# Kernel tuning notes

Measured on AMD Instinct MI355X. Metric: run time of the kernel, lower is better.

The kernel has to match this reference:

```python
import jax, jax.numpy as jnp
import numpy as np

B, N, D, H = 4, 8192, 1024, 16
HD = D // H  # head dim 64
EPS = 1e-5


def setup_inputs() -> dict:
    key = jax.random.key(0)
    ks = jax.random.split(key, 12)
    s = 1.0 / np.sqrt(D)
    return {
        "query": jax.random.normal(ks[0], (B, N, D), jnp.float32),
        "Wq": jax.random.normal(ks[1], (D, D), jnp.float32) * s,
        "bq": jax.random.normal(ks[2], (D,), jnp.float32) * 0.01,
        "Wk": jax.random.normal(ks[3], (D, D), jnp.float32) * s,
        "bk": jax.random.normal(ks[4], (D,), jnp.float32) * 0.01,
        "Wv": jax.random.normal(ks[5], (D, D), jnp.float32) * s,
        "bv": jax.random.normal(ks[6], (D,), jnp.float32) * 0.01,
        "Wu": jax.random.normal(ks[7], (D, D), jnp.float32) * s,
        "bu": jax.random.normal(ks[8], (D,), jnp.float32) * 0.01,
        "Wo": jax.random.normal(ks[9], (D, D), jnp.float32) * s,
        "bo": jax.random.normal(ks[10], (D,), jnp.float32) * 0.01,
        "ln_w": jnp.ones((D,), jnp.float32),
        "ln_b": jnp.zeros((D,), jnp.float32),
    }


def _abs_clamp(t, min_mag=0.01, max_mag=100.0):
    return jnp.clip(jnp.abs(t), min_mag, max_mag) * jnp.sign(t)


def _heads(x):  # [b, n, h*d] -> [b, h, n, d]
    b, n, _ = x.shape
    return x.reshape(b, n, H, HD).transpose(0, 2, 1, 3)


def reference(query, Wq, bq, Wk, bk, Wv, bv, Wu, bu, Wo, bo, ln_w, ln_b):
    q = jax.nn.relu(_heads(query @ Wq + bq))  # [b,h,n,d]
    k = jax.nn.relu(_heads(query @ Wk + bk))
    v = _heads(query @ Wv + bv)
    u = query @ Wu + bu  # [b,n,D]
    # global linear-attention reduction: kv[b,h,d,e] = sum_n k v
    kv = jnp.einsum('bhnd,bhne->bhde', k, v)
    kv = _abs_clamp(kv)
    out = jnp.einsum('bhnd,bhde->bhne', q, kv)  # [b,h,n,d]
    out = out.transpose(0, 2, 1, 3).reshape(query.shape)  # [b,n,D]
    # LayerNorm over last dim
    mu = jnp.mean(out, axis=-1, keepdims=True)
    var = jnp.var(out, axis=-1, keepdims=True)
    out = (out - mu) * jax.lax.rsqrt(var + EPS) * ln_w + ln_b
    out = u * out
    return out @ Wo + bo
```

## Files before the change

### kernel.cpp

```cpp
#include <hip/hip_runtime.h>

#define M_TOT 32768

typedef float f32x4 __attribute__((ext_vector_type(4)));
typedef short s16x8 __attribute__((ext_vector_type(8)));

#define AS1(p) ((__attribute__((address_space(1))) void*)(p))
#define AS3(p) ((__attribute__((address_space(3))) void*)(p))

#define BARRIER() asm volatile("s_barrier" ::: "memory")
#define VMCNT4() asm volatile("s_waitcnt vmcnt(4)" ::: "memory")
#define VMCNT2() asm volatile("s_waitcnt vmcnt(2)" ::: "memory")
#define VMCNT0() asm volatile("s_waitcnt vmcnt(0)" ::: "memory")

__device__ __forceinline__ short f2bf(float f) {
    unsigned u = __builtin_bit_cast(unsigned, f);
    u += 0x7fffu + ((u >> 16) & 1u);
    return (short)(u >> 16);
}
__device__ __forceinline__ float bf2f(short s) {
    unsigned u = ((unsigned)(unsigned short)s) << 16;
    return __builtin_bit_cast(float, u);
}

__global__ void conv_x(const float* __restrict__ x, short* __restrict__ y) {
    const size_t nchunk = (size_t)M_TOT * 1024 / 8;
    const size_t stride = (size_t)gridDim.x * blockDim.x;
    for (size_t c = (size_t)blockIdx.x * blockDim.x + threadIdx.x; c < nchunk; c += stride) {
        const float4* src = (const float4*)(x + c * 8);
        float4 a = src[0], b = src[1];
        s16x8 r;
        r[0] = f2bf(a.x); r[1] = f2bf(a.y); r[2] = f2bf(a.z); r[3] = f2bf(a.w);
        r[4] = f2bf(b.x); r[5] = f2bf(b.y); r[6] = f2bf(b.z); r[7] = f2bf(b.w);
        *(s16x8*)(y + c * 8) = r;
    }
}

__global__ void conv_w(const float* __restrict__ Wq, const float* __restrict__ Wk,
                       const float* __restrict__ Wv, const float* __restrict__ Wu,
                       const float* __restrict__ Wo, short* __restrict__ Wcat) {
    const int c = blockIdx.x * 256 + threadIdx.x;
    const int np = c >> 8;
    const int k0 = (c & 255) << 2;
    const float* W = (np < 1024) ? Wq : (np < 2048) ? Wk : (np < 3072) ? Wv
                   : (np < 4096) ? Wu : Wo;
    const int n = np & 1023;
    short4 r;
    r.x = f2bf(W[(size_t)(k0 + 0) * 1024 + n]);
    r.y = f2bf(W[(size_t)(k0 + 1) * 1024 + n]);
    r.z = f2bf(W[(size_t)(k0 + 2) * 1024 + n]);
    r.w = f2bf(W[(size_t)(k0 + 3) * 1024 + n]);
    *(short4*)(Wcat + (size_t)np * 1024 + k0) = r;
}

__global__ void conv_bias(const float* __restrict__ bq, const float* __restrict__ bk,
                          const float* __restrict__ bv, const float* __restrict__ bu,
                          const float* __restrict__ bo, float* __restrict__ bcat) {
    const int i = blockIdx.x * 256 + threadIdx.x;
    const float* b = (i < 1024) ? bq : (i < 2048) ? bk : (i < 3072) ? bv
                   : (i < 4096) ? bu : bo;
    bcat[i] = b[i & 1023];
}

template <int MODE>
__global__ __launch_bounds__(512, 2) void gemm8(
        const short* __restrict__ A, const short* __restrict__ W,
        const float* __restrict__ bias,
        short* __restrict__ qb, short* __restrict__ ktb,
        short* __restrict__ vtb, short* __restrict__ ub,
        float* __restrict__ outb) {
    extern __shared__ char lds[];
    const int tid = threadIdx.x;
    const int wave = tid >> 6, lane = tid & 63;
    const int r16 = lane & 15, g = lane >> 4;
    const int moff = (wave >> 2) << 7;
    const int noff = (wave & 3) << 6;

    const int nwg = (MODE == 0) ? 2048 : 512;
    const int NB = (MODE == 0) ? 16 : 4;
    const int bid = blockIdx.x;
    const int swz = (bid & 7) * (nwg >> 3) + (bid >> 3);
    const int mblk = swz / NB, nblk = swz % NB;
    const int row0 = mblk << 8, col0 = nblk << 8;

    const int rswz = r16 & 7;
    const int ck0 = (g ^ rswz) << 4;
    const int ck1 = ((4 + g) ^ rswz) << 4;
    const int rowbA = (moff + r16) << 7;
    const int rowbB = (noff + r16) << 7;

    const char* baseA = (const char*)A + (size_t)(row0 + wave * 8 + (lane >> 3)) * 2048
                        + (((lane & 7) ^ ((lane >> 3) & 7)) << 4);
    const char* baseB = (const char*)W + (size_t)(col0 + wave * 8 + (lane >> 3)) * 2048
                        + (((lane & 7) ^ ((lane >> 3) & 7)) << 4);

#define STG(BASE, J, T, DST)                                                   \
    __builtin_amdgcn_global_load_lds(                                          \
        AS1((BASE) + (size_t)(J) * 131072 + (size_t)(T) * 128),                \
        AS3((DST) + (J) * 8192 + wave * 1024), 16, 0, 0)

#define RDA(V, M, BUFA) {                                                      \
    (V)[0] = *(const s16x8*)((BUFA) + rowbA + (M) * 2048 + ck0);               \
    (V)[1] = *(const s16x8*)((BUFA) + rowbA + (M) * 2048 + ck1); }

#define RDB(V, N, BUFB) {                                                      \
    (V)[0] = *(const s16x8*)((BUFB) + rowbB + (N) * 2048 + ck0);               \
    (V)[1] = *(const s16x8*)((BUFB) + rowbB + (N) * 2048 + ck1); }

#define MF16(P)                                                                \
    _Pragma("unroll") for (int n = 0; n < 4; ++n) {                            \
        acc[2*(P)][n]   = __builtin_amdgcn_mfma_f32_16x16x32_bf16(afr[0][0], bfr[n][0], acc[2*(P)][n], 0, 0, 0);   \
        acc[2*(P)+1][n] = __builtin_amdgcn_mfma_f32_16x16x32_bf16(afr[1][0], bfr[n][0], acc[2*(P)+1][n], 0, 0, 0); \
        acc[2*(P)][n]   = __builtin_amdgcn_mfma_f32_16x16x32_bf16(afr[0][1], bfr[n][1], acc[2*(P)][n], 0, 0, 0);   \
        acc[2*(P)+1][n] = __builtin_amdgcn_mfma_f32_16x16x32_bf16(afr[1][1], bfr[n][1], acc[2*(P)+1][n], 0, 0, 0); \
    }

#define TILE(T, DOSTAGE, TR2, TR4) {                                           \
    char* bA_ = lds + ((T) & 1) * 65536; char* bB_ = bA_ + 32768;              \
    char* sA_ = lds + (((T) + 1) & 1) * 65536; char* sB_ = sA_ + 32768;        \
    s16x8 afr[2][2];                                                           \
    if (DOSTAGE) { STG(baseB, 0, (T) + 1, sB_); STG(baseB, 1, (T) + 1, sB_); } \
    _Pragma("unroll") for (int n = 0; n < 4; ++n) RDB(bfr[n], n, bB_);         \
    RDA(afr[0], 0, bA_); RDA(afr[1], 1, bA_);                                  \
    BARRIER(); __builtin_amdgcn_s_setprio(1); MF16(0);                         \
    __builtin_amdgcn_s_setprio(0); BARRIER();                                  \
    if (DOSTAGE) { STG(baseB, 2, (T) + 1, sB_); STG(baseB, 3, (T) + 1, sB_); } \
    RDA(afr[0], 2, bA_); RDA(afr[1], 3, bA_);                                  \
    BARRIER(); __builtin_amdgcn_s_setprio(1); MF16(1);                         \
    __builtin_amdgcn_s_setprio(0); TR2; BARRIER();                             \
    if (DOSTAGE) { STG(baseA, 0, (T) + 1, sA_); STG(baseA, 2, (T) + 1, sA_); } \
    RDA(afr[0], 4, bA_); RDA(afr[1], 5, bA_);                                  \
    BARRIER(); __builtin_amdgcn_s_setprio(1); MF16(2);                         \
    __builtin_amdgcn_s_setprio(0); BARRIER();                                  \
    if (DOSTAGE) { STG(baseA, 1, (T) + 1, sA_); STG(baseA, 3, (T) + 1, sA_); } \
    RDA(afr[0], 6, bA_); RDA(afr[1], 7, bA_);                                  \
    BARRIER(); __builtin_amdgcn_s_setprio(1); MF16(3);                         \
    __builtin_amdgcn_s_setprio(0); TR4; BARRIER();                             \
}

    f32x4 acc[8][4] = {};
    s16x8 bfr[4][2];

    STG(baseB, 0, 0, lds + 32768); STG(baseB, 1, 0, lds + 32768);
    STG(baseB, 2, 0, lds + 32768); STG(baseB, 3, 0, lds + 32768);
    STG(baseA, 0, 0, lds);         STG(baseA, 2, 0, lds);
    STG(baseA, 1, 0, lds);         STG(baseA, 3, 0, lds);
    VMCNT2();
    BARRIER();

    #pragma unroll 1
    for (int t = 0; t < 15; ++t) TILE(t, true, VMCNT4(), VMCNT2());
    TILE(15, false, VMCNT0(), (void)0);

    const int rj = (lane >> 4) << 2;
    if (MODE == 1) {
        #pragma unroll
        for (int n = 0; n < 4; ++n) {
            const int gn = col0 + noff + n * 16 + r16;
            const float bv = bias[gn];
            #pragma unroll
            for (int m = 0; m < 8; ++m) {
                const int gm0 = row0 + moff + m * 16 + rj;
                #pragma unroll
                for (int j = 0; j < 4; ++j)
                    outb[(size_t)(gm0 + j) * 1024 + gn] = acc[m][n][j] + bv;
            }
        }
    } else {
        const int seg = col0 >> 10;
        if (seg == 0 || seg == 3) {
            short* dst = (seg == 0) ? qb : ub;
            const bool do_relu = (seg == 0);
            #pragma unroll
            for (int n = 0; n < 4; ++n) {
                const int gn = col0 + noff + n * 16 + r16;
                const int f = gn & 1023;
                const float bv = bias[gn];
                #pragma unroll
                for (int m = 0; m < 8; ++m) {
                    const int gm0 = row0 + moff + m * 16 + rj;
                    #pragma unroll
                    for (int j = 0; j < 4; ++j) {
                        float val = acc[m][n][j] + bv;
                        if (do_relu) val = fmaxf(val, 0.0f);
                        dst[(size_t)(gm0 + j) * 1024 + f] = f2bf(val);
                    }
                }
            }
        } else {
            short* dst = (seg == 1) ? ktb : vtb;
            const bool do_relu = (seg == 1);
            #pragma unroll
            for (int n = 0; n < 4; ++n) {
                const int gn = col0 + noff + n * 16 + r16;
                const int hd = gn & 1023;
                const float bv = bias[gn];
                #pragma unroll
                for (int m = 0; m < 8; ++m) {
                    const int gm0 = row0 + moff + m * 16 + rj;
                    const int b = gm0 >> 13;
                    const int ntok = gm0 & 8191;
                    float v0 = acc[m][n][0] + bv, v1 = acc[m][n][1] + bv;
                    float v2 = acc[m][n][2] + bv, v3 = acc[m][n][3] + bv;
                    if (do_relu) {
                        v0 = fmaxf(v0, 0.0f); v1 = fmaxf(v1, 0.0f);
                        v2 = fmaxf(v2, 0.0f); v3 = fmaxf(v3, 0.0f);
                    }
                    short4 pk;
                    pk.x = f2bf(v0); pk.y = f2bf(v1); pk.z = f2bf(v2); pk.w = f2bf(v3);
                    *(short4*)(dst + ((size_t)(b * 1024 + hd)) * 8192 + ntok) = pk;
                }
            }
        }
    }
#undef TILE
#undef MF16
#undef RDB
#undef RDA
#undef STG
}

__global__ __launch_bounds__(64) void kv_partial(const short* __restrict__ ktb,
                                                 const short* __restrict__ vtb,
                                                 float* __restrict__ kvp) {
    const int slice = blockIdx.x;
    const int bh = blockIdx.y;
    const int lane = threadIdx.x;
    const int r16 = lane & 15;
    const short* kb = ktb + (size_t)bh * 64 * 8192;
    const short* vb = vtb + (size_t)bh * 64 * 8192;
    const int n0 = slice << 8;
    f32x4 acc[4][4] = {};
    for (int s = 0; s < 8; ++s) {
        const int nk = n0 + (s << 5) + ((lane >> 4) << 3);
        s16x8 af[4], bf[4];
        #pragma unroll
        for (int m = 0; m < 4; ++m) af[m] = *(const s16x8*)(kb + (size_t)(m * 16 + r16) * 8192 + nk);
        #pragma unroll
        for (int n = 0; n < 4; ++n) bf[n] = *(const s16x8*)(vb + (size_t)(n * 16 + r16) * 8192 + nk);
        #pragma unroll
        for (int m = 0; m < 4; ++m)
            #pragma unroll
            for (int n = 0; n < 4; ++n)
                acc[m][n] = __builtin_amdgcn_mfma_f32_16x16x32_bf16(af[m], bf[n], acc[m][n], 0, 0, 0);
    }
    float* dst = kvp + ((size_t)slice * 64 + bh) * 4096;
    const int rj = (lane >> 4) << 2;
    #pragma unroll
    for (int m = 0; m < 4; ++m)
        #pragma unroll
        for (int n = 0; n < 4; ++n)
            #pragma unroll
            for (int j = 0; j < 4; ++j)
                dst[(size_t)(m * 16 + rj + j) * 64 + n * 16 + r16] = acc[m][n][j];
}

__global__ void kv_reduce(const float* __restrict__ kvp, short* __restrict__ kvt) {
    const int bh = blockIdx.x;
    for (int i = threadIdx.x; i < 4096; i += 256) {
        float s = 0.0f;
        #pragma unroll 8
        for (int sl = 0; sl < 32; ++sl)
            s += kvp[((size_t)sl * 64 + bh) * 4096 + i];
        float a = fabsf(s);
        float cmag = fminf(fmaxf(a, 0.01f), 100.0f);
        float r = (s > 0.0f) ? cmag : ((s < 0.0f) ? -cmag : 0.0f);
        const int d = i >> 6, e = i & 63;
        kvt[(size_t)bh * 4096 + e * 64 + d] = f2bf(r);
    }
}

__global__ __launch_bounds__(256) void qkv_out(const short* __restrict__ qb,
                                               const short* __restrict__ kvt,
                                               float* __restrict__ ob) {
    const int bh = blockIdx.y;
    const int b = bh >> 4, h = bh & 15;
    const int tid = threadIdx.x;
    const int wave = tid >> 6, lane = tid & 63;
    const int r16 = lane & 15;
    const size_t mbase = (size_t)b * 8192 + ((size_t)blockIdx.x << 8) + (wave << 6);
    const short* kvb = kvt + (size_t)bh * 4096;
    f32x4 acc[4][4] = {};
    #pragma unroll
    for (int s = 0; s < 2; ++s) {
        const int kq2 = (s << 5) + ((lane >> 4) << 3);
        s16x8 af[4], bf[4];
        #pragma unroll
        for (int m = 0; m < 4; ++m)
            af[m] = *(const s16x8*)(qb + (mbase + m * 16 + r16) * 1024 + h * 64 + kq2);
        #pragma unroll
        for (int n = 0; n < 4; ++n)
            bf[n] = *(const s16x8*)(kvb + (n * 16 + r16) * 64 + kq2);
        #pragma unroll
        for (int m = 0; m < 4; ++m)
            #pragma unroll
            for (int n = 0; n < 4; ++n)
                acc[m][n] = __builtin_amdgcn_mfma_f32_16x16x32_bf16(af[m], bf[n], acc[m][n], 0, 0, 0);
    }
    const int rj = (lane >> 4) << 2;
    #pragma unroll
    for (int m = 0; m < 4; ++m)
        #pragma unroll
        for (int n = 0; n < 4; ++n)
            #pragma unroll
            for (int j = 0; j < 4; ++j)
                ob[(mbase + m * 16 + rj + j) * 1024 + h * 64 + n * 16 + r16] = acc[m][n][j];
}

__global__ __launch_bounds__(256) void ln_mul(const float* __restrict__ ob,
                                              const short* __restrict__ ub,
                                              const float* __restrict__ lnw,
                                              const float* __restrict__ lnb,
                                              short* __restrict__ yb) {
    const int row = blockIdx.x;
    const int tid = threadIdx.x;
    const float4 v = ((const float4*)(ob + (size_t)row * 1024))[tid];
    float s = v.x + v.y + v.z + v.w;
    float sq = v.x * v.x + v.y * v.y + v.z * v.z + v.w * v.w;
    #pragma unroll
    for (int off = 32; off > 0; off >>= 1) {
        s += __shfl_down(s, off);
        sq += __shfl_down(sq, off);
    }
    __shared__ float ls[4], lq[4];
    const int wave = tid >> 6, lane = tid & 63;
    if (lane == 0) { ls[wave] = s; lq[wave] = sq; }
    __syncthreads();
    const float S = ls[0] + ls[1] + ls[2] + ls[3];
    const float SQ = lq[0] + lq[1] + lq[2] + lq[3];
    const float mu = S * (1.0f / 1024.0f);
    const float var = SQ * (1.0f / 1024.0f) - mu * mu;
    const float rs = rsqrtf(var + 1e-5f);
    const short4 uu = ((const short4*)(ub + (size_t)row * 1024))[tid];
    const float4 w = ((const float4*)lnw)[tid];
    const float4 bb = ((const float4*)lnb)[tid];
    short4 o;
    o.x = f2bf(bf2f(uu.x) * ((v.x - mu) * rs * w.x + bb.x));
    o.y = f2bf(bf2f(uu.y) * ((v.y - mu) * rs * w.y + bb.y));
    o.z = f2bf(bf2f(uu.z) * ((v.z - mu) * rs * w.z + bb.z));
    o.w = f2bf(bf2f(uu.w) * ((v.w - mu) * rs * w.w + bb.w));
    ((short4*)(yb + (size_t)row * 1024))[tid] = o;
}

extern "C" void kernel_launch(void* const* d_in, const int* in_sizes, int n_in,
                              void* d_out, int out_size, void* d_ws, size_t ws_size,
                              hipStream_t stream) {
    (void)in_sizes; (void)n_in; (void)out_size;
    const float* query = (const float*)d_in[0];
    const float* Wq = (const float*)d_in[1];
    const float* bq = (const float*)d_in[2];
    const float* Wk = (const float*)d_in[3];
    const float* bk = (const float*)d_in[4];
    const float* Wv = (const float*)d_in[5];
    const float* bv = (const float*)d_in[6];
    const float* Wu = (const float*)d_in[7];
    const float* bu = (const float*)d_in[8];
    const float* Wo = (const float*)d_in[9];
    const float* bo = (const float*)d_in[10];
    const float* lnw = (const float*)d_in[11];
    const float* lnb = (const float*)d_in[12];
    float* out = (float*)d_out;
    char* ws = (char*)d_ws;
    if (ws_size < 380129280u) return;

    short* Xb   = (short*)(ws);
    short* Wcat = (short*)(ws + 67108864);
    float* bcat = (float*)(ws + 77594624);
    short* qb   = (short*)(ws + 77615104);
    short* ktb  = (short*)(ws + 144723968);
    short* vtb  = (short*)(ws + 211832832);
    short* ub   = (short*)(ws + 278941696);
    float* kvp  = (float*)(ws + 346050560);
    short* kvt  = (short*)(ws + 379604992);
    float* ob   = (float*)(ws + 144723968);
    short* yb   = Xb;

    hipFuncSetAttribute(reinterpret_cast<const void*>(&gemm8<0>),
                        hipFuncAttributeMaxDynamicSharedMemorySize, 131072);
    hipFuncSetAttribute(reinterpret_cast<const void*>(&gemm8<1>),
                        hipFuncAttributeMaxDynamicSharedMemorySize, 131072);

    conv_x<<<2048, 256, 0, stream>>>(query, Xb);
    conv_w<<<5120, 256, 0, stream>>>(Wq, Wk, Wv, Wu, Wo, Wcat);
    conv_bias<<<20, 256, 0, stream>>>(bq, bk, bv, bu, bo, bcat);
    gemm8<0><<<2048, 512, 131072, stream>>>(Xb, Wcat, bcat, qb, ktb, vtb, ub, nullptr);
    kv_partial<<<dim3(32, 64), 64, 0, stream>>>(ktb, vtb, kvp);
    kv_reduce<<<64, 256, 0, stream>>>(kvp, kvt);
    qkv_out<<<dim3(32, 64), 256, 0, stream>>>(qb, kvt, ob);
    ln_mul<<<32768, 256, 0, stream>>>(ob, ub, lnw, lnb, yb);
    gemm8<1><<<512, 512, 131072, stream>>>(yb, Wcat + (size_t)4096 * 1024, bcat + 4096,
                                           nullptr, nullptr, nullptr, nullptr, out);
}
```

Measured before the change: 600.5 us.

## Fuse q·kv product with LayerNorm and reduce kv partials inside blocks

Replaces the separate qkv_out and ln_mul kernels with one qkv_ln kernel. It computes each row's attention output per head with MFMA twice, once for the LayerNorm statistics and once for normalization, and then multiplies by u through an LDS transpose. This removes the fp32 round trip of the 128MB output buffer through global memory, at the cost of doing the small q·kv matmul twice. kv_partial now uses 4 waves per block that reduce their partial sums in LDS, which cuts the partial slices from 32 to 8. The MFMA issue order in the gemm macro is also reordered by k-step.

```diff
diff --git a/kernel.cpp b/kernel.cpp
--- a/kernel.cpp
+++ b/kernel.cpp
@@ -108,12 +108,11 @@
     (V)[1] = *(const s16x8*)((BUFB) + rowbB + (N) * 2048 + ck1); }
 
 #define MF16(P)                                                                \
-    _Pragma("unroll") for (int n = 0; n < 4; ++n) {                            \
-        acc[2*(P)][n]   = __builtin_amdgcn_mfma_f32_16x16x32_bf16(afr[0][0], bfr[n][0], acc[2*(P)][n], 0, 0, 0);   \
-        acc[2*(P)+1][n] = __builtin_amdgcn_mfma_f32_16x16x32_bf16(afr[1][0], bfr[n][0], acc[2*(P)+1][n], 0, 0, 0); \
-        acc[2*(P)][n]   = __builtin_amdgcn_mfma_f32_16x16x32_bf16(afr[0][1], bfr[n][1], acc[2*(P)][n], 0, 0, 0);   \
-        acc[2*(P)+1][n] = __builtin_amdgcn_mfma_f32_16x16x32_bf16(afr[1][1], bfr[n][1], acc[2*(P)+1][n], 0, 0, 0); \
-    }
+    _Pragma("unroll") for (int kk = 0; kk < 2; ++kk)                           \
+        _Pragma("unroll") for (int n = 0; n < 4; ++n) {                        \
+            acc[2*(P)][n]   = __builtin_amdgcn_mfma_f32_16x16x32_bf16(afr[0][kk], bfr[n][kk], acc[2*(P)][n], 0, 0, 0);   \
+            acc[2*(P)+1][n] = __builtin_amdgcn_mfma_f32_16x16x32_bf16(afr[1][kk], bfr[n][kk], acc[2*(P)+1][n], 0, 0, 0); \
+        }
 
 #define TILE(T, DOSTAGE, TR2, TR4) {                                           \
     char* bA_ = lds + ((T) & 1) * 65536; char* bB_ = bA_ + 32768;              \
@@ -220,16 +219,17 @@
 #undef STG
 }
 
-__global__ __launch_bounds__(64) void kv_partial(const short* __restrict__ ktb,
-                                                 const short* __restrict__ vtb,
-                                                 float* __restrict__ kvp) {
+__global__ __launch_bounds__(256) void kv_partial(const short* __restrict__ ktb,
+                                                  const short* __restrict__ vtb,
+                                                  float* __restrict__ kvp) {
+    __shared__ float red[4][4096];
     const int slice = blockIdx.x;
     const int bh = blockIdx.y;
-    const int lane = threadIdx.x;
+    const int wave = threadIdx.x >> 6, lane = threadIdx.x & 63;
     const int r16 = lane & 15;
     const short* kb = ktb + (size_t)bh * 64 * 8192;
     const short* vb = vtb + (size_t)bh * 64 * 8192;
-    const int n0 = slice << 8;
+    const int n0 = (slice << 10) + (wave << 8);
     f32x4 acc[4][4] = {};
     for (int s = 0; s < 8; ++s) {
         const int nk = n0 + (s << 5) + ((lane >> 4) << 3);
@@ -244,7 +244,6 @@
             for (int n = 0; n < 4; ++n)
                 acc[m][n] = __builtin_amdgcn_mfma_f32_16x16x32_bf16(af[m], bf[n], acc[m][n], 0, 0, 0);
     }
-    float* dst = kvp + ((size_t)slice * 64 + bh) * 4096;
     const int rj = (lane >> 4) << 2;
     #pragma unroll
     for (int m = 0; m < 4; ++m)
@@ -252,15 +251,26 @@
         for (int n = 0; n < 4; ++n)
             #pragma unroll
             for (int j = 0; j < 4; ++j)
-                dst[(size_t)(m * 16 + rj + j) * 64 + n * 16 + r16] = acc[m][n][j];
+                red[wave][(m * 16 + rj + j) * 64 + n * 16 + r16] = acc[m][n][j];
+    __syncthreads();
+    float* dst = kvp + ((size_t)slice * 64 + bh) * 4096;
+    const int i0 = threadIdx.x * 16;
+    #pragma unroll
+    for (int e = 0; e < 16; e += 4) {
+        f32x4 a0 = *(const f32x4*)&red[0][i0 + e];
+        f32x4 a1 = *(const f32x4*)&red[1][i0 + e];
+        f32x4 a2 = *(const f32x4*)&red[2][i0 + e];
+        f32x4 a3 = *(const f32x4*)&red[3][i0 + e];
+        *(f32x4*)&dst[i0 + e] = (a0 + a1) + (a2 + a3);
+    }
 }
 
 __global__ void kv_reduce(const float* __restrict__ kvp, short* __restrict__ kvt) {
     const int bh = blockIdx.x;
     for (int i = threadIdx.x; i < 4096; i += 256) {
         float s = 0.0f;
-        #pragma unroll 8
-        for (int sl = 0; sl < 32; ++sl)
+        #pragma unroll
+        for (int sl = 0; sl < 8; ++sl)
             s += kvp[((size_t)sl * 64 + bh) * 4096 + i];
         float a = fabsf(s);
         float cmag = fminf(fmaxf(a, 0.01f), 100.0f);
@@ -270,76 +280,93 @@
     }
 }
 
-__global__ __launch_bounds__(256) void qkv_out(const short* __restrict__ qb,
-                                               const short* __restrict__ kvt,
-                                               float* __restrict__ ob) {
-    const int bh = blockIdx.y;
-    const int b = bh >> 4, h = bh & 15;
-    const int tid = threadIdx.x;
-    const int wave = tid >> 6, lane = tid & 63;
-    const int r16 = lane & 15;
-    const size_t mbase = (size_t)b * 8192 + ((size_t)blockIdx.x << 8) + (wave << 6);
-    const short* kvb = kvt + (size_t)bh * 4096;
-    f32x4 acc[4][4] = {};
-    #pragma unroll
-    for (int s = 0; s < 2; ++s) {
-        const int kq2 = (s << 5) + ((lane >> 4) << 3);
-        s16x8 af[4], bf[4];
-        #pragma unroll
-        for (int m = 0; m < 4; ++m)
-            af[m] = *(const s16x8*)(qb + (mbase + m * 16 + r16) * 1024 + h * 64 + kq2);
-        #pragma unroll
-        for (int n = 0; n < 4; ++n)
-            bf[n] = *(const s16x8*)(kvb + (n * 16 + r16) * 64 + kq2);
-        #pragma unroll
-        for (int m = 0; m < 4; ++m)
-            #pragma unroll
-            for (int n = 0; n < 4; ++n)
-                acc[m][n] = __builtin_amdgcn_mfma_f32_16x16x32_bf16(af[m], bf[n], acc[m][n], 0, 0, 0);
-    }
-    const int rj = (lane >> 4) << 2;
-    #pragma unroll
-    for (int m = 0; m < 4; ++m)
-        #pragma unroll
-        for (int n = 0; n < 4; ++n)
-            #pragma unroll
-            for (int j = 0; j < 4; ++j)
-                ob[(mbase + m * 16 + rj + j) * 1024 + h * 64 + n * 16 + r16] = acc[m][n][j];
-}
-
-__global__ __launch_bounds__(256) void ln_mul(const float* __restrict__ ob,
+__global__ __launch_bounds__(256) void qkv_ln(const short* __restrict__ qb,
+                                              const short* __restrict__ kvt,
                                               const short* __restrict__ ub,
                                               const float* __restrict__ lnw,
                                               const float* __restrict__ lnb,
                                               short* __restrict__ yb) {
-    const int row = blockIdx.x;
-    const int tid = threadIdx.x;
-    const float4 v = ((const float4*)(ob + (size_t)row * 1024))[tid];
-    float s = v.x + v.y + v.z + v.w;
-    float sq = v.x * v.x + v.y * v.y + v.z * v.z + v.w * v.w;
+    __shared__ short tr[4][1024];
+    const int wave = threadIdx.x >> 6, lane = threadIdx.x & 63;
+    const int r16 = lane & 15, g = lane >> 4;
+    const size_t rowB = (size_t)blockIdx.x * 64 + wave * 16;
+    const int bh0 = (int)((rowB >> 13) << 4);
+    const short* qrow = qb + (rowB + r16) * 1024 + g * 8;
+
+    float s[4] = {0, 0, 0, 0}, sq[4] = {0, 0, 0, 0};
+    for (int h = 0; h < 16; ++h) {
+        const short* kvb = kvt + (size_t)(bh0 + h) * 4096 + g * 8;
+        f32x4 a4[4] = {};
+        #pragma unroll
+        for (int kk = 0; kk < 2; ++kk) {
+            const s16x8 af = *(const s16x8*)(qrow + h * 64 + kk * 32);
+            #pragma unroll
+            for (int n = 0; n < 4; ++n) {
+                const s16x8 bf = *(const s16x8*)(kvb + (n * 16 + r16) * 64 + kk * 32);
+                a4[n] = __builtin_amdgcn_mfma_f32_16x16x32_bf16(af, bf, a4[n], 0, 0, 0);
+            }
+        }
+        #pragma unroll
+        for (int n = 0; n < 4; ++n)
+            #pragma unroll
+            for (int j = 0; j < 4; ++j) {
+                const float v = a4[n][j];
+                s[j] += v; sq[j] += v * v;
+            }
+    }
     #pragma unroll
-    for (int off = 32; off > 0; off >>= 1) {
-        s += __shfl_down(s, off);
-        sq += __shfl_down(sq, off);
-    }
-    __shared__ float ls[4], lq[4];
-    const int wave = tid >> 6, lane = tid & 63;
-    if (lane == 0) { ls[wave] = s; lq[wave] = sq; }
-    __syncthreads();
-    const float S = ls[0] + ls[1] + ls[2] + ls[3];
-    const float SQ = lq[0] + lq[1] + lq[2] + lq[3];
-    const float mu = S * (1.0f / 1024.0f);
-    const float var = SQ * (1.0f / 1024.0f) - mu * mu;
-    const float rs = rsqrtf(var + 1e-5f);
-    const short4 uu = ((const short4*)(ub + (size_t)row * 1024))[tid];
-    const float4 w = ((const float4*)lnw)[tid];
-    const float4 bb = ((const float4*)lnb)[tid];
-    short4 o;
-    o.x = f2bf(bf2f(uu.x) * ((v.x - mu) * rs * w.x + bb.x));
-    o.y = f2bf(bf2f(uu.y) * ((v.y - mu) * rs * w.y + bb.y));
-    o.z = f2bf(bf2f(uu.z) * ((v.z - mu) * rs * w.z + bb.z));
-    o.w = f2bf(bf2f(uu.w) * ((v.w - mu) * rs * w.w + bb.w));
-    ((short4*)(yb + (size_t)row * 1024))[tid] = o;
+    for (int j = 0; j < 4; ++j) {
+        #pragma unroll
+        for (int mk = 1; mk < 16; mk <<= 1) {
+            s[j] += __shfl_xor(s[j], mk);
+            sq[j] += __shfl_xor(sq[j], mk);
+        }
+    }
+    float mu[4], rs[4];
+    #pragma unroll
+    for (int j = 0; j < 4; ++j) {
+        mu[j] = s[j] * (1.0f / 1024.0f);
+        const float var = sq[j] * (1.0f / 1024.0f) - mu[j] * mu[j];
+        rs[j] = rsqrtf(var + 1e-5f);
+    }
+
+    short* trw = &tr[wave][0];
+    const int rdr = lane >> 3;
+    const int c0 = (lane & 7) * 8;
+    for (int h = 0; h < 16; ++h) {
+        const short* kvb = kvt + (size_t)(bh0 + h) * 4096 + g * 8;
+        f32x4 a4[4] = {};
+        #pragma unroll
+        for (int kk = 0; kk < 2; ++kk) {
+            const s16x8 af = *(const s16x8*)(qrow + h * 64 + kk * 32);
+            #pragma unroll
+            for (int n = 0; n < 4; ++n) {
+                const s16x8 bf = *(const s16x8*)(kvb + (n * 16 + r16) * 64 + kk * 32);
+                a4[n] = __builtin_amdgcn_mfma_f32_16x16x32_bf16(af, bf, a4[n], 0, 0, 0);
+            }
+        }
+        #pragma unroll
+        for (int n = 0; n < 4; ++n) {
+            const float lw = lnw[h * 64 + n * 16 + r16];
+            const float lb = lnb[h * 64 + n * 16 + r16];
+            #pragma unroll
+            for (int j = 0; j < 4; ++j) {
+                const float val = (a4[n][j] - mu[j]) * rs[j] * lw + lb;
+                trw[(g * 4 + j) * 64 + ((n ^ g) * 16 + r16)] = f2bf(val);
+            }
+        }
+        #pragma unroll
+        for (int p = 0; p < 2; ++p) {
+            const int r = rdr + p * 8;
+            const s16x8 t = *(const s16x8*)&trw[r * 64 + (((c0 >> 4) ^ (r >> 2)) * 16) + (c0 & 15)];
+            const s16x8 uu = *(const s16x8*)(ub + (rowB + r) * 1024 + h * 64 + c0);
+            s16x8 o;
+            #pragma unroll
+            for (int e = 0; e < 8; ++e)
+                o[e] = f2bf(bf2f(t[e]) * bf2f(uu[e]));
+            *(s16x8*)(yb + (rowB + r) * 1024 + h * 64 + c0) = o;
+        }
+    }
 }
 
 extern "C" void kernel_launch(void* const* d_in, const int* in_sizes, int n_in,
@@ -372,7 +399,6 @@
     short* ub   = (short*)(ws + 278941696);
     float* kvp  = (float*)(ws + 346050560);
     short* kvt  = (short*)(ws + 379604992);
-    float* ob   = (float*)(ws + 144723968);
     short* yb   = Xb;
 
     hipFuncSetAttribute(reinterpret_cast<const void*>(&gemm8<0>),
@@ -384,10 +410,9 @@
     conv_w<<<5120, 256, 0, stream>>>(Wq, Wk, Wv, Wu, Wo, Wcat);
     conv_bias<<<20, 256, 0, stream>>>(bq, bk, bv, bu, bo, bcat);
     gemm8<0><<<2048, 512, 131072, stream>>>(Xb, Wcat, bcat, qb, ktb, vtb, ub, nullptr);
-    kv_partial<<<dim3(32, 64), 64, 0, stream>>>(ktb, vtb, kvp);
+    kv_partial<<<dim3(8, 64), 256, 0, stream>>>(ktb, vtb, kvp);
     kv_reduce<<<64, 256, 0, stream>>>(kvp, kvt);
-    qkv_out<<<dim3(32, 64), 256, 0, stream>>>(qb, kvt, ob);
-    ln_mul<<<32768, 256, 0, stream>>>(ob, ub, lnw, lnb, yb);
+    qkv_ln<<<512, 256, 0, stream>>>(qb, kvt, ub, lnw, lnb, yb);
     gemm8<1><<<512, 512, 131072, stream>>>(yb, Wcat + (size_t)4096 * 1024, bcat + 4096,
                                            nullptr, nullptr, nullptr, nullptr, out);
 }
```

Result: faster. 557.8 us (-7.1%).
